# Optimization experiments

Hardware: AMD Instinct MI355X
Metric: run time of the kernel (lower is better)

## Reference

```python
import jax, jax.numpy as jnp
import numpy as np

EMBED_DIM = 1024
NUM_HEADS = 16
HEAD_DIM = 64
B, S = 4, 2048


def setup_inputs() -> dict:
    key = jax.random.key(0)
    ks = jax.random.split(key, 5)
    std = 0.02
    x = jax.random.normal(ks[0], (B, S, EMBED_DIM), dtype=jnp.float32)
    Wq = std * jax.random.normal(ks[1], (NUM_HEADS, EMBED_DIM, HEAD_DIM), dtype=jnp.float32)
    Wk = std * jax.random.normal(ks[2], (NUM_HEADS, EMBED_DIM, HEAD_DIM), dtype=jnp.float32)
    Wv = std * jax.random.normal(ks[3], (NUM_HEADS, EMBED_DIM, HEAD_DIM), dtype=jnp.float32)
    Wo = std * jax.random.normal(ks[4], (NUM_HEADS, HEAD_DIM, EMBED_DIM), dtype=jnp.float32)
    bq = jnp.zeros((NUM_HEADS, HEAD_DIM), dtype=jnp.float32)
    bk = jnp.zeros((NUM_HEADS, HEAD_DIM), dtype=jnp.float32)
    bv = jnp.zeros((NUM_HEADS, HEAD_DIM), dtype=jnp.float32)
    bo = jnp.zeros((EMBED_DIM,), dtype=jnp.float32)
    return {"x": x, "Wq": Wq, "bq": bq, "Wk": Wk, "bk": bk,
            "Wv": Wv, "bv": bv, "Wo": Wo, "bo": bo}


def reference(x, Wq, bq, Wk, bk, Wv, bv, Wo, bo):
    # q,k,v: [b, s, n, h]
    q = jnp.einsum('bsd,ndh->bsnh', x, Wq) + bq
    k = jnp.einsum('bsd,ndh->bsnh', x, Wk) + bk
    v = jnp.einsum('bsd,ndh->bsnh', x, Wv) + bv
    scale = 1.0 / (HEAD_DIM ** 0.5)
    # non-causal full attention matrix [b, n, s, t]
    attn = jnp.einsum('bsnh,btnh->bnst', q, k) * scale
    attn = jax.nn.softmax(attn, axis=-1)
    after = jnp.einsum('bnst,btnh->bsnh', attn, v)
    out = jnp.einsum('bsnh,nhd->bsd', after, Wo) + bo
    return out
```

## Files before the change

### kernel.cpp

```cpp
#include <hip/hip_runtime.h>

typedef __bf16 bf16;
typedef bf16 bf16x8 __attribute__((ext_vector_type(8)));
typedef bf16 bf16x4 __attribute__((ext_vector_type(4)));
typedef float f32x4 __attribute__((ext_vector_type(4)));

constexpr int Bb = 4, Ss = 2048, Dd = 1024, NH = 16, HD = 64;
constexpr int BS = Bb * Ss;
constexpr float CSC = 0.18033688011112042f;
constexpr int PST = 68;

__device__ __forceinline__ int sw(int row, int col) {
  return (row << 6) + (col ^ ((row & 7) << 3));
}

__device__ __forceinline__ void g2l16(const bf16* g, bf16* l) {
  __builtin_amdgcn_global_load_lds(
      (const __attribute__((address_space(1))) void*)g,
      (__attribute__((address_space(3))) void*)l, 16, 0, 0);
}

__global__ void convert_x(const float* __restrict__ x, bf16* __restrict__ xb) {
  int o = (blockIdx.x * 256 + threadIdx.x) * 4;
  f32x4 v = *(const f32x4*)&x[o];
  bf16x4 r = {(bf16)v[0], (bf16)v[1], (bf16)v[2], (bf16)v[3]};
  *(bf16x4*)&xb[o] = r;
}

__global__ void prep(const float* __restrict__ Wq, const float* __restrict__ Wk,
                     const float* __restrict__ Wv, const float* __restrict__ Wo,
                     const float* __restrict__ bq, const float* __restrict__ bk,
                     const float* __restrict__ bv,
                     bf16* __restrict__ WT_all, bf16* __restrict__ WoT,
                     float* __restrict__ bias_all) {
  __shared__ bf16 Ts[64 * 72];
  const int t = threadIdx.x;
  const int sel = blockIdx.y;
  if (sel < 3) {
    const float* W = (sel == 0) ? Wq : (sel == 1) ? Wk : Wv;
    float scale = (sel == 0) ? CSC : 1.0f;
    int head = blockIdx.x >> 4, dt = blockIdx.x & 15;
    const float* src = W + head * 65536 + dt * 64 * 64;
#pragma unroll
    for (int i = 0; i < 4; ++i) {
      int idx = i * 256 + t;
      int dr = idx >> 4, hc = (idx & 15) * 4;
      f32x4 v = *(const f32x4*)&src[dr * 64 + hc];
#pragma unroll
      for (int k = 0; k < 4; ++k) Ts[(hc + k) * 72 + dr] = (bf16)(v[k] * scale);
    }
    __syncthreads();
    bf16* dst = WT_all + (size_t)sel * 1048576 + (size_t)(head * 64) * 1024 + dt * 64;
#pragma unroll
    for (int i = 0; i < 2; ++i) {
      int idx = i * 256 + t;
      int hr = idx >> 3, ch = (idx & 7) * 8;
      *(bf16x8*)&dst[(size_t)hr * 1024 + ch] = *(const bf16x8*)&Ts[hr * 72 + ch];
    }
  } else if (sel == 3) {
    int ct = blockIdx.x >> 4, dt = blockIdx.x & 15;
    const float* src = Wo + (size_t)(ct * 64) * 1024 + dt * 64;
#pragma unroll
    for (int i = 0; i < 4; ++i) {
      int idx = i * 256 + t;
      int cr = idx >> 4, dc = (idx & 15) * 4;
      f32x4 v = *(const f32x4*)&src[(size_t)cr * 1024 + dc];
#pragma unroll
      for (int k = 0; k < 4; ++k) Ts[(dc + k) * 72 + cr] = (bf16)v[k];
    }
    __syncthreads();
    bf16* dst = WoT + (size_t)(dt * 64) * 1024 + ct * 64;
#pragma unroll
    for (int i = 0; i < 2; ++i) {
      int idx = i * 256 + t;
      int dr = idx >> 3, ch = (idx & 7) * 8;
      *(bf16x8*)&dst[(size_t)dr * 1024 + ch] = *(const bf16x8*)&Ts[dr * 72 + ch];
    }
  } else if (blockIdx.x == 0) {
    for (int j = t; j < 3072; j += 256) {
      int s2 = j >> 10;
      const float* bb = (s2 == 0) ? bq : (s2 == 1) ? bk : bv;
      bias_all[j] = bb[j & 1023] * (s2 == 0 ? CSC : 1.0f);
    }
  }
}

__device__ __forceinline__ void gemm_core(const bf16* __restrict__ A,
                                          const bf16* __restrict__ BT,
                                          int m0, int n0, bf16* As, bf16* Bs,
                                          f32x4 (&acc)[4][4]) {
  const int t = threadIdx.x;
  const int l = t & 63, q = l >> 4, lm = l & 15;
  const int w = t >> 6, wm = w & 1, wn = w >> 1;
  int ro[4], co[4];
#pragma unroll
  for (int i = 0; i < 4; ++i) {
    int o = i * 256 + t;
    ro[i] = o >> 3;
    co[i] = ((o & 7) ^ ((o >> 3) & 7)) << 3;
  }
  const int lbase = (t & 192) * 8;
  for (int k0 = 0; k0 < 1024; k0 += 64) {
    __syncthreads();
#pragma unroll
    for (int i = 0; i < 4; ++i)
      g2l16(&A[(size_t)(m0 + ro[i]) * 1024 + k0 + co[i]], &As[i * 2048 + lbase]);
#pragma unroll
    for (int i = 0; i < 4; ++i)
      g2l16(&BT[(size_t)(n0 + ro[i]) * 1024 + k0 + co[i]], &Bs[i * 2048 + lbase]);
    __syncthreads();
#pragma unroll
    for (int kh = 0; kh < 2; ++kh) {
      bf16x8 a[4], b[4];
#pragma unroll
      for (int i = 0; i < 4; ++i)
        a[i] = *(const bf16x8*)&As[sw(wm * 64 + i * 16 + lm, kh * 32 + q * 8)];
#pragma unroll
      for (int i = 0; i < 4; ++i)
        b[i] = *(const bf16x8*)&Bs[sw(wn * 64 + i * 16 + lm, kh * 32 + q * 8)];
#pragma unroll
      for (int mt = 0; mt < 4; ++mt)
#pragma unroll
        for (int nt = 0; nt < 4; ++nt)
          acc[mt][nt] = __builtin_amdgcn_mfma_f32_16x16x32_bf16(a[mt], b[nt], acc[mt][nt], 0, 0, 0);
    }
  }
}

__global__ __launch_bounds__(256) void gemm_qkv(const bf16* __restrict__ xb,
                                                const bf16* __restrict__ WT,
                                                const float* __restrict__ bias_all,
                                                bf16* __restrict__ QKb,
                                                bf16* __restrict__ VTb) {
  __shared__ __align__(16) bf16 As[128 * 64];
  __shared__ __align__(16) bf16 Bs[128 * 64];
  const int bid = blockIdx.x;
  const int t = threadIdx.x;
  const int l = t & 63, q = l >> 4, lm = l & 15;
  const int w = t >> 6, wm = w & 1, wn = w >> 1;
  const bool vmode = bid >= 1024;
  int m0, n0;
  const bf16 *A, *BT;
  if (!vmode) {
    int xcd = bid & 7, idx = bid >> 3;
    m0 = (idx >> 1) * 128;
    n0 = (xcd * 2 + (idx & 1)) * 128;
    A = xb; BT = WT;
  } else {
    int b2 = bid - 1024;
    int xcd = b2 & 7, idx = b2 >> 3;
    m0 = (idx >> 3) * 128;
    n0 = (xcd * 8 + (idx & 7)) * 128;
    A = WT + (size_t)2048 * 1024; BT = xb;
  }
  f32x4 acc[4][4] = {};
  gemm_core(A, BT, m0, n0, As, Bs, acc);
  if (vmode) {
#pragma unroll
    for (int nt = 0; nt < 4; ++nt) {
      int sg = n0 + wn * 64 + nt * 16 + lm;
      size_t sb = (size_t)(sg >> 11) * 2097152 + (sg & 2047);
#pragma unroll
      for (int mt = 0; mt < 4; ++mt)
#pragma unroll
        for (int r = 0; r < 4; ++r) {
          int m = m0 + wm * 64 + mt * 16 + q * 4 + r;
          VTb[sb + (size_t)(m >> 6) * 131072 + (size_t)(m & 63) * 2048] =
              (bf16)(acc[mt][nt][r] + bias_all[2048 + m]);
        }
    }
  } else {
#pragma unroll
    for (int nt = 0; nt < 4; ++nt) {
      int col = n0 + wn * 64 + nt * 16 + lm;
      float bb = bias_all[col];
#pragma unroll
      for (int mt = 0; mt < 4; ++mt) {
        int row = m0 + wm * 64 + mt * 16 + q * 4;
#pragma unroll
        for (int r = 0; r < 4; ++r)
          QKb[(size_t)(row + r) * 2048 + col] = (bf16)(acc[mt][nt][r] + bb);
      }
    }
  }
}

__global__ __launch_bounds__(256) void gemm_out(const bf16* __restrict__ after,
                                                const bf16* __restrict__ WoT,
                                                const float* __restrict__ bo,
                                                float* __restrict__ out) {
  __shared__ __align__(16) bf16 As[128 * 64];
  __shared__ __align__(16) bf16 Bs[128 * 64];
  const int bid = blockIdx.x;
  const int t = threadIdx.x;
  const int l = t & 63, q = l >> 4, lm = l & 15;
  const int w = t >> 6, wm = w & 1, wn = w >> 1;
  const int xcd = bid & 7, idx = bid >> 3;
  const int n0 = xcd * 128, m0 = idx * 128;
  f32x4 acc[4][4] = {};
  gemm_core(after, WoT, m0, n0, As, Bs, acc);
#pragma unroll
  for (int nt = 0; nt < 4; ++nt) {
    int col = n0 + wn * 64 + nt * 16 + lm;
    float bb = bo[col];
#pragma unroll
    for (int mt = 0; mt < 4; ++mt) {
      int row = m0 + wm * 64 + mt * 16 + q * 4;
#pragma unroll
      for (int r = 0; r < 4; ++r)
        out[(size_t)(row + r) * 1024 + col] = acc[mt][nt][r] + bb;
    }
  }
}

__global__ __launch_bounds__(256, 3) void attn(const bf16* __restrict__ QK,
                                               const bf16* __restrict__ VT,
                                               bf16* __restrict__ after) {
  __shared__ __align__(16) bf16 Ks[2][64 * 64];
  __shared__ __align__(16) bf16 Vs[2][64 * 64];
  __shared__ __align__(16) bf16 Ps[128 * PST];
  const int t = threadIdx.x;
  const int l = t & 63, q = l >> 4, lm = l & 15, w = t >> 6;
  const int f = blockIdx.x;
  const int bn = (f & 7) | ((f >> 7) << 3);
  const int s0 = ((f >> 3) & 15) * 128;
  const int b = bn >> 4, n = bn & 15;
  const bf16* Qb = QK + (size_t)(b * 2048) * 2048 + n * 64;
  const bf16* Kb = Qb + 1024;
  const bf16* Vtb = VT + (size_t)bn * 131072;
  int ro[4], co[4];
#pragma unroll
  for (int i = 0; i < 4; ++i) {
    int o = i * 256 + t;
    ro[i] = o >> 3;
    co[i] = ((o & 7) ^ ((o >> 3) & 7)) << 3;
  }
  const int lbase = (t & 192) * 8;
  bf16* Kflat = &Ks[0][0];
#pragma unroll
  for (int i = 0; i < 4; ++i)
    g2l16(&Qb[(size_t)(s0 + ro[i]) * 2048 + co[i]], Kflat + i * 2048 + lbase);
  __syncthreads();
  bf16x8 qa[2][2];
#pragma unroll
  for (int mt = 0; mt < 2; ++mt)
#pragma unroll
    for (int kh = 0; kh < 2; ++kh)
      qa[mt][kh] = *(const bf16x8*)&Kflat[sw(w * 32 + mt * 16 + lm, kh * 32 + q * 8)];
  __syncthreads();
#pragma unroll
  for (int i = 0; i < 2; ++i) {
    g2l16(&Kb[(size_t)ro[i] * 2048 + co[i]], &Ks[0][i * 2048 + lbase]);
    g2l16(&Vtb[(size_t)ro[i] * 2048 + co[i]], &Vs[0][i * 2048 + lbase]);
  }
  f32x4 o_acc[2][4] = {};
  f32x4 rsum[2] = {};
  const bf16x8 ones = {(bf16)1.f, (bf16)1.f, (bf16)1.f, (bf16)1.f,
                       (bf16)1.f, (bf16)1.f, (bf16)1.f, (bf16)1.f};
  for (int rd = 0; rd < 32; ++rd) {
    const int cur = rd & 1;
    __syncthreads();
    if (rd < 31) {
      int t0n = (rd + 1) * 64, nb = cur ^ 1;
#pragma unroll
      for (int i = 0; i < 2; ++i) {
        g2l16(&Kb[(size_t)(t0n + ro[i]) * 2048 + co[i]], &Ks[nb][i * 2048 + lbase]);
        g2l16(&Vtb[(size_t)ro[i] * 2048 + t0n + co[i]], &Vs[nb][i * 2048 + lbase]);
      }
    }
    f32x4 sc[2][4] = {};
#pragma unroll
    for (int kh = 0; kh < 2; ++kh) {
      bf16x8 kb[4];
#pragma unroll
      for (int c = 0; c < 4; ++c)
        kb[c] = *(const bf16x8*)&Ks[cur][sw(c * 16 + lm, kh * 32 + q * 8)];
#pragma unroll
      for (int mt = 0; mt < 2; ++mt)
#pragma unroll
        for (int c = 0; c < 4; ++c)
          sc[mt][c] = __builtin_amdgcn_mfma_f32_16x16x32_bf16(kb[c], qa[mt][kh], sc[mt][c], 0, 0, 0);
    }
#pragma unroll
    for (int mt = 0; mt < 2; ++mt) {
      int srow = w * 32 + mt * 16 + lm;
#pragma unroll
      for (int c = 0; c < 4; ++c) {
        bf16x4 pk;
#pragma unroll
        for (int r = 0; r < 4; ++r)
          pk[r] = (bf16)__builtin_amdgcn_exp2f(sc[mt][c][r]);
        *(bf16x4*)&Ps[srow * PST + (c * 4 + q) * 4] = pk;
      }
    }
#pragma unroll
    for (int kh = 0; kh < 2; ++kh) {
      bf16x8 vb[4];
#pragma unroll
      for (int c = 0; c < 4; ++c)
        vb[c] = *(const bf16x8*)&Vs[cur][sw(c * 16 + lm, kh * 32 + q * 8)];
      bf16x8 pa[2];
#pragma unroll
      for (int mt = 0; mt < 2; ++mt) {
        int srow = w * 32 + mt * 16 + lm;
        bf16x4 lo = *(const bf16x4*)&Ps[srow * PST + (kh * 8 + q * 2) * 4];
        bf16x4 hi = *(const bf16x4*)&Ps[srow * PST + (kh * 8 + q * 2) * 4 + 4];
        pa[mt] = __builtin_shufflevector(lo, hi, 0, 1, 2, 3, 4, 5, 6, 7);
      }
#pragma unroll
      for (int mt = 0; mt < 2; ++mt)
        rsum[mt] = __builtin_amdgcn_mfma_f32_16x16x32_bf16(pa[mt], ones, rsum[mt], 0, 0, 0);
#pragma unroll
      for (int mt = 0; mt < 2; ++mt)
#pragma unroll
        for (int c = 0; c < 4; ++c)
          o_acc[mt][c] = __builtin_amdgcn_mfma_f32_16x16x32_bf16(pa[mt], vb[c], o_acc[mt][c], 0, 0, 0);
    }
  }
#pragma unroll
  for (int mt = 0; mt < 2; ++mt)
#pragma unroll
    for (int r = 0; r < 4; ++r) {
      float inv = 1.f / rsum[mt][r];
      int srow = s0 + w * 32 + mt * 16 + q * 4 + r;
      size_t base = (size_t)(b * 2048 + srow) * 1024 + n * 64;
#pragma unroll
      for (int c = 0; c < 4; ++c)
        after[base + c * 16 + lm] = (bf16)(o_acc[mt][c][r] * inv);
    }
}

extern "C" void kernel_launch(void* const* d_in, const int* in_sizes, int n_in,
                              void* d_out, int out_size, void* d_ws, size_t ws_size,
                              hipStream_t stream) {
  const float* x  = (const float*)d_in[0];
  const float* Wq = (const float*)d_in[1];
  const float* bq = (const float*)d_in[2];
  const float* Wk = (const float*)d_in[3];
  const float* bk = (const float*)d_in[4];
  const float* Wv = (const float*)d_in[5];
  const float* bv = (const float*)d_in[6];
  const float* Wo = (const float*)d_in[7];
  const float* bo = (const float*)d_in[8];
  float* out = (float*)d_out;

  bf16* WT_all    = (bf16*)d_ws;
  bf16* WoT       = WT_all + (size_t)3072 * 1024;
  float* bias_all = (float*)(WoT + (size_t)1024 * 1024);
  bf16* xb        = (bf16*)(bias_all + 4096);
  bf16* QKb       = xb + (size_t)BS * Dd;
  bf16* VTb       = QKb + (size_t)BS * 2048;
  bf16* after     = VTb + (size_t)Bb * NH * HD * Ss;

  convert_x<<<dim3(BS * Dd / 1024), dim3(256), 0, stream>>>(x, xb);
  prep<<<dim3(256, 5), dim3(256), 0, stream>>>(Wq, Wk, Wv, Wo, bq, bk, bv,
                                               WT_all, WoT, bias_all);
  gemm_qkv<<<dim3(1536), dim3(256), 0, stream>>>(xb, WT_all, bias_all, QKb, VTb);
  attn<<<dim3(1024), dim3(256), 0, stream>>>(QKb, VTb, after);
  gemm_out<<<dim3(512), dim3(256), 0, stream>>>(after, WoT, bo, out);
}
```

Before: 277.0 us.

## Use 32x32x16 MFMA in attention with register-shuffled P, merge prep kernels

Rewrites the attention inner loop to use 32x32x16 bf16 MFMAs. The exponentiated scores are passed to the PV product through cross-lane shuffles instead of an LDS round trip, and the ones-MFMA row sum is replaced by a scalar per-lane sum. This removes the P shared buffer and its barriers, lowering LDS use, and raises the launch-bounds occupancy target to 4. The x conversion kernel is also folded into the weight prep kernel to save a launch, at the cost of many idle blocks in the second grid row.

```diff
diff --git a/kernel.cpp b/kernel.cpp
--- a/kernel.cpp
+++ b/kernel.cpp
@@ -3,12 +3,15 @@
 typedef __bf16 bf16;
 typedef bf16 bf16x8 __attribute__((ext_vector_type(8)));
 typedef bf16 bf16x4 __attribute__((ext_vector_type(4)));
+typedef bf16 bf16x2 __attribute__((ext_vector_type(2)));
 typedef float f32x4 __attribute__((ext_vector_type(4)));
+typedef float f32x16 __attribute__((ext_vector_type(16)));
+typedef unsigned int u32;
+typedef u32 u32x4 __attribute__((ext_vector_type(4)));
 
 constexpr int Bb = 4, Ss = 2048, Dd = 1024, NH = 16, HD = 64;
 constexpr int BS = Bb * Ss;
 constexpr float CSC = 0.18033688011112042f;
-constexpr int PST = 68;
 
 __device__ __forceinline__ int sw(int row, int col) {
   return (row << 6) + (col ^ ((row & 7) << 3));
@@ -20,14 +23,13 @@
       (__attribute__((address_space(3))) void*)l, 16, 0, 0);
 }
 
-__global__ void convert_x(const float* __restrict__ x, bf16* __restrict__ xb) {
-  int o = (blockIdx.x * 256 + threadIdx.x) * 4;
-  f32x4 v = *(const f32x4*)&x[o];
-  bf16x4 r = {(bf16)v[0], (bf16)v[1], (bf16)v[2], (bf16)v[3]};
-  *(bf16x4*)&xb[o] = r;
-}
-
-__global__ void prep(const float* __restrict__ Wq, const float* __restrict__ Wk,
+__device__ __forceinline__ u32 pkbf(float a, float b) {
+  bf16x2 v = {(bf16)a, (bf16)b};
+  return __builtin_bit_cast(u32, v);
+}
+
+__global__ void prep(const float* __restrict__ x, bf16* __restrict__ xb,
+                     const float* __restrict__ Wq, const float* __restrict__ Wk,
                      const float* __restrict__ Wv, const float* __restrict__ Wo,
                      const float* __restrict__ bq, const float* __restrict__ bk,
                      const float* __restrict__ bv,
@@ -35,11 +37,27 @@
                      float* __restrict__ bias_all) {
   __shared__ bf16 Ts[64 * 72];
   const int t = threadIdx.x;
-  const int sel = blockIdx.y;
+  if (blockIdx.y == 0) {
+    int o = (blockIdx.x * 256 + t) * 4;
+    f32x4 v = *(const f32x4*)&x[o];
+    bf16x4 r = {(bf16)v[0], (bf16)v[1], (bf16)v[2], (bf16)v[3]};
+    *(bf16x4*)&xb[o] = r;
+    return;
+  }
+  if (blockIdx.x > 1024) return;
+  if (blockIdx.x == 1024) {
+    for (int j = t; j < 3072; j += 256) {
+      int s2 = j >> 10;
+      const float* bb = (s2 == 0) ? bq : (s2 == 1) ? bk : bv;
+      bias_all[j] = bb[j & 1023] * (s2 == 0 ? CSC : 1.0f);
+    }
+    return;
+  }
+  const int sel = blockIdx.x >> 8, bx = blockIdx.x & 255;
   if (sel < 3) {
     const float* W = (sel == 0) ? Wq : (sel == 1) ? Wk : Wv;
     float scale = (sel == 0) ? CSC : 1.0f;
-    int head = blockIdx.x >> 4, dt = blockIdx.x & 15;
+    int head = bx >> 4, dt = bx & 15;
     const float* src = W + head * 65536 + dt * 64 * 64;
 #pragma unroll
     for (int i = 0; i < 4; ++i) {
@@ -57,8 +75,8 @@
       int hr = idx >> 3, ch = (idx & 7) * 8;
       *(bf16x8*)&dst[(size_t)hr * 1024 + ch] = *(const bf16x8*)&Ts[hr * 72 + ch];
     }
-  } else if (sel == 3) {
-    int ct = blockIdx.x >> 4, dt = blockIdx.x & 15;
+  } else {
+    int ct = bx >> 4, dt = bx & 15;
     const float* src = Wo + (size_t)(ct * 64) * 1024 + dt * 64;
 #pragma unroll
     for (int i = 0; i < 4; ++i) {
@@ -75,12 +93,6 @@
       int idx = i * 256 + t;
       int dr = idx >> 3, ch = (idx & 7) * 8;
       *(bf16x8*)&dst[(size_t)dr * 1024 + ch] = *(const bf16x8*)&Ts[dr * 72 + ch];
-    }
-  } else if (blockIdx.x == 0) {
-    for (int j = t; j < 3072; j += 256) {
-      int s2 = j >> 10;
-      const float* bb = (s2 == 0) ? bq : (s2 == 1) ? bk : bv;
-      bias_all[j] = bb[j & 1023] * (s2 == 0 ? CSC : 1.0f);
     }
   }
 }
@@ -213,14 +225,14 @@
   }
 }
 
-__global__ __launch_bounds__(256, 3) void attn(const bf16* __restrict__ QK,
+__global__ __launch_bounds__(256, 4) void attn(const bf16* __restrict__ QK,
                                                const bf16* __restrict__ VT,
                                                bf16* __restrict__ after) {
   __shared__ __align__(16) bf16 Ks[2][64 * 64];
   __shared__ __align__(16) bf16 Vs[2][64 * 64];
-  __shared__ __align__(16) bf16 Ps[128 * PST];
-  const int t = threadIdx.x;
-  const int l = t & 63, q = l >> 4, lm = l & 15, w = t >> 6;
+  const int t = threadIdx.x;
+  const int l = t & 63, w = t >> 6;
+  const int lh = l & 31, H = l >> 5;
   const int f = blockIdx.x;
   const int bn = (f & 7) | ((f >> 7) << 3);
   const int s0 = ((f >> 3) & 15) * 128;
@@ -241,22 +253,18 @@
   for (int i = 0; i < 4; ++i)
     g2l16(&Qb[(size_t)(s0 + ro[i]) * 2048 + co[i]], Kflat + i * 2048 + lbase);
   __syncthreads();
-  bf16x8 qa[2][2];
-#pragma unroll
-  for (int mt = 0; mt < 2; ++mt)
-#pragma unroll
-    for (int kh = 0; kh < 2; ++kh)
-      qa[mt][kh] = *(const bf16x8*)&Kflat[sw(w * 32 + mt * 16 + lm, kh * 32 + q * 8)];
+  bf16x8 qb[4];
+#pragma unroll
+  for (int ks = 0; ks < 4; ++ks)
+    qb[ks] = *(const bf16x8*)&Kflat[sw(w * 32 + lh, ks * 16 + H * 8)];
   __syncthreads();
 #pragma unroll
   for (int i = 0; i < 2; ++i) {
     g2l16(&Kb[(size_t)ro[i] * 2048 + co[i]], &Ks[0][i * 2048 + lbase]);
     g2l16(&Vtb[(size_t)ro[i] * 2048 + co[i]], &Vs[0][i * 2048 + lbase]);
   }
-  f32x4 o_acc[2][4] = {};
-  f32x4 rsum[2] = {};
-  const bf16x8 ones = {(bf16)1.f, (bf16)1.f, (bf16)1.f, (bf16)1.f,
-                       (bf16)1.f, (bf16)1.f, (bf16)1.f, (bf16)1.f};
+  f32x16 o_acc[2] = {};
+  float rs = 0.f;
   for (int rd = 0; rd < 32; ++rd) {
     const int cur = rd & 1;
     __syncthreads();
@@ -268,66 +276,51 @@
         g2l16(&Vtb[(size_t)ro[i] * 2048 + t0n + co[i]], &Vs[nb][i * 2048 + lbase]);
       }
     }
-    f32x4 sc[2][4] = {};
-#pragma unroll
-    for (int kh = 0; kh < 2; ++kh) {
-      bf16x8 kb[4];
-#pragma unroll
-      for (int c = 0; c < 4; ++c)
-        kb[c] = *(const bf16x8*)&Ks[cur][sw(c * 16 + lm, kh * 32 + q * 8)];
-#pragma unroll
-      for (int mt = 0; mt < 2; ++mt)
-#pragma unroll
-        for (int c = 0; c < 4; ++c)
-          sc[mt][c] = __builtin_amdgcn_mfma_f32_16x16x32_bf16(kb[c], qa[mt][kh], sc[mt][c], 0, 0, 0);
-    }
-#pragma unroll
-    for (int mt = 0; mt < 2; ++mt) {
-      int srow = w * 32 + mt * 16 + lm;
-#pragma unroll
-      for (int c = 0; c < 4; ++c) {
-        bf16x4 pk;
-#pragma unroll
-        for (int r = 0; r < 4; ++r)
-          pk[r] = (bf16)__builtin_amdgcn_exp2f(sc[mt][c][r]);
-        *(bf16x4*)&Ps[srow * PST + (c * 4 + q) * 4] = pk;
-      }
-    }
-#pragma unroll
-    for (int kh = 0; kh < 2; ++kh) {
-      bf16x8 vb[4];
-#pragma unroll
-      for (int c = 0; c < 4; ++c)
-        vb[c] = *(const bf16x8*)&Vs[cur][sw(c * 16 + lm, kh * 32 + q * 8)];
-      bf16x8 pa[2];
-#pragma unroll
-      for (int mt = 0; mt < 2; ++mt) {
-        int srow = w * 32 + mt * 16 + lm;
-        bf16x4 lo = *(const bf16x4*)&Ps[srow * PST + (kh * 8 + q * 2) * 4];
-        bf16x4 hi = *(const bf16x4*)&Ps[srow * PST + (kh * 8 + q * 2) * 4 + 4];
-        pa[mt] = __builtin_shufflevector(lo, hi, 0, 1, 2, 3, 4, 5, 6, 7);
-      }
-#pragma unroll
-      for (int mt = 0; mt < 2; ++mt)
-        rsum[mt] = __builtin_amdgcn_mfma_f32_16x16x32_bf16(pa[mt], ones, rsum[mt], 0, 0, 0);
-#pragma unroll
-      for (int mt = 0; mt < 2; ++mt)
-#pragma unroll
-        for (int c = 0; c < 4; ++c)
-          o_acc[mt][c] = __builtin_amdgcn_mfma_f32_16x16x32_bf16(pa[mt], vb[c], o_acc[mt][c], 0, 0, 0);
-    }
-  }
-#pragma unroll
-  for (int mt = 0; mt < 2; ++mt)
-#pragma unroll
-    for (int r = 0; r < 4; ++r) {
-      float inv = 1.f / rsum[mt][r];
-      int srow = s0 + w * 32 + mt * 16 + q * 4 + r;
-      size_t base = (size_t)(b * 2048 + srow) * 1024 + n * 64;
-#pragma unroll
-      for (int c = 0; c < 4; ++c)
-        after[base + c * 16 + lm] = (bf16)(o_acc[mt][c][r] * inv);
-    }
+#pragma unroll
+    for (int tt = 0; tt < 2; ++tt) {
+      f32x16 sc = {};
+#pragma unroll
+      for (int ks = 0; ks < 4; ++ks) {
+        bf16x8 kb = *(const bf16x8*)&Ks[cur][sw(tt * 32 + lh, ks * 16 + H * 8)];
+        sc = __builtin_amdgcn_mfma_f32_32x32x16_bf16(kb, qb[ks], sc, 0, 0, 0);
+      }
+      u32 pk[8], xx[8];
+#pragma unroll
+      for (int i = 0; i < 8; ++i) {
+        float p0 = __builtin_amdgcn_exp2f(sc[2 * i]);
+        float p1 = __builtin_amdgcn_exp2f(sc[2 * i + 1]);
+        rs += p0 + p1;
+        pk[i] = pkbf(p0, p1);
+      }
+#pragma unroll
+      for (int i = 0; i < 8; ++i) xx[i] = __shfl_xor((int)pk[i], 32);
+#pragma unroll
+      for (int ks2 = 0; ks2 < 2; ++ks2) {
+        u32x4 av;
+        av[0] = H ? xx[ks2 * 4 + 2] : pk[ks2 * 4 + 0];
+        av[1] = H ? xx[ks2 * 4 + 3] : pk[ks2 * 4 + 1];
+        av[2] = H ? pk[ks2 * 4 + 2] : xx[ks2 * 4 + 0];
+        av[3] = H ? pk[ks2 * 4 + 3] : xx[ks2 * 4 + 1];
+        bf16x8 pa = __builtin_bit_cast(bf16x8, av);
+#pragma unroll
+        for (int ht = 0; ht < 2; ++ht) {
+          bf16x8 vb = *(const bf16x8*)&Vs[cur][sw(ht * 32 + lh, tt * 32 + ks2 * 16 + H * 8)];
+          o_acc[ht] = __builtin_amdgcn_mfma_f32_32x32x16_bf16(pa, vb, o_acc[ht], 0, 0, 0);
+        }
+      }
+    }
+  }
+  rs += __shfl_xor(rs, 32);
+  float inv = 1.f / rs;
+#pragma unroll
+  for (int r = 0; r < 16; ++r) {
+    int sl = (r & 3) + 8 * (r >> 2) + 4 * H;
+    float invr = __shfl(inv, sl);
+    size_t base = (size_t)(b * 2048 + s0 + w * 32 + sl) * 1024 + n * 64;
+#pragma unroll
+    for (int ht = 0; ht < 2; ++ht)
+      after[base + ht * 32 + lh] = (bf16)(o_acc[ht][r] * invr);
+  }
 }
 
 extern "C" void kernel_launch(void* const* d_in, const int* in_sizes, int n_in,
@@ -352,9 +345,8 @@
   bf16* VTb       = QKb + (size_t)BS * 2048;
   bf16* after     = VTb + (size_t)Bb * NH * HD * Ss;
 
-  convert_x<<<dim3(BS * Dd / 1024), dim3(256), 0, stream>>>(x, xb);
-  prep<<<dim3(256, 5), dim3(256), 0, stream>>>(Wq, Wk, Wv, Wo, bq, bk, bv,
-                                               WT_all, WoT, bias_all);
+  prep<<<dim3(8192, 2), dim3(256), 0, stream>>>(x, xb, Wq, Wk, Wv, Wo, bq, bk, bv,
+                                                WT_all, WoT, bias_all);
   gemm_qkv<<<dim3(1536), dim3(256), 0, stream>>>(xb, WT_all, bias_all, QKb, VTb);
   attn<<<dim3(1024), dim3(256), 0, stream>>>(QKb, VTb, after);
   gemm_out<<<dim3(512), dim3(256), 0, stream>>>(after, WoT, bo, out);
```

Result: slower. 285.6 us (+3.1%).
